# Kernel optimization log

Measured on AMD Instinct MI355X. Metric: run time of the kernel, lower is better.

## Reference

```python
import jax, jax.numpy as jnp
import numpy as np

S = 1024   # speakers_per_batch
U = 64     # utterances_per_speaker
E = 256    # model_embedding_size


def setup_inputs() -> dict:
    key = jax.random.key(0)
    k1, _ = jax.random.split(key)
    # embeds as produced by forward(): relu'd then L2-normalized rows
    raw = jax.nn.relu(jax.random.normal(k1, (S * U, E), dtype=jnp.float32))
    embeds = raw / (jnp.linalg.norm(raw, axis=1, keepdims=True) + 1e-12)
    return {
        "embeds": embeds,
        "similarity_weight": jnp.array([10.0], dtype=jnp.float32),
        "similarity_bias": jnp.array([-5.0], dtype=jnp.float32),
    }


def reference(embeds, similarity_weight, similarity_bias):
    e = embeds.reshape(S, U, E)                      # [S,U,E]
    # inclusive centroids (per speaker)
    c_incl = jnp.mean(e, axis=1)                     # [S,E]
    incl_norm = jnp.linalg.norm(c_incl, axis=1)      # [S]
    # exclusive centroids (leave-one-out per utterance)
    c_excl = (jnp.sum(e, axis=1, keepdims=True) - e) / (U - 1)  # [S,U,E]
    excl_norm = jnp.linalg.norm(c_excl, axis=2)      # [S,U]
    # off-diagonal (k != j): cosine vs inclusive centroid of speaker k
    sim = jnp.einsum('jue,ke->juk', e, c_incl) / incl_norm       # [S,U,S]
    # diagonal (k == j): cosine vs own exclusive centroid
    diag = jnp.einsum('jue,jue->ju', e, c_excl) / excl_norm      # [S,U]
    idx = jnp.arange(S)
    sim = sim.at[idx, :, idx].set(diag)
    sim = sim * similarity_weight[0] + similarity_bias[0]
    # cross-entropy against ground truth speaker ids
    logits = sim.reshape(S * U, S)                   # [SU,S]
    gt = jnp.repeat(jnp.arange(S), U)                # [SU]
    logp = jax.nn.log_softmax(logits, axis=-1)
    loss = -jnp.mean(jnp.take_along_axis(logp, gt[:, None], axis=1))
    preds = jnp.argmax(logits, axis=1)
    accuracy = jnp.mean((preds == gt).astype(jnp.float32))
    return loss, accuracy
```

## Files before the change

### kernel.cpp

```cpp
#include <hip/hip_runtime.h>
#include <math.h>

#define NS 1024
#define NU 64
#define NE 256

typedef __attribute__((ext_vector_type(4))) float f32x4;

__device__ static inline unsigned int pk4_fp8(float a, float b, float c,
                                              float d) {
  int r = 0;
  r = __builtin_amdgcn_cvt_pk_fp8_f32(a, b, r, false);
  r = __builtin_amdgcn_cvt_pk_fp8_f32(c, d, r, true);
  return (unsigned int)r;
}


__global__ __launch_bounds__(256) void centroid_kernel(
    const float* __restrict__ embeds, unsigned int* __restrict__ Cb,
    float* __restrict__ normsum, float* __restrict__ ssumG,
    unsigned int* __restrict__ pmaxG, float* __restrict__ out) {
  int k = blockIdx.x;
  int t = threadIdx.x;
  if (t < 64) {
    ssumG[k * 64 + t] = 0.f;
    pmaxG[k * 64 + t] = 0u;
  }
  int wave = t >> 6, e4 = t & 63;
  const float4* base =
      (const float4*)(embeds + (size_t)k * NU * NE) + wave * 16 * 64 + e4;
  float4 s = {0.f, 0.f, 0.f, 0.f};
#pragma unroll
  for (int i = 0; i < 16; ++i) {
    float4 v = base[i * 64];
    s.x += v.x; s.y += v.y; s.z += v.z; s.w += v.w;
  }
  __shared__ float4 ps[4][64];
  ps[wave][e4] = s;
  __syncthreads();
  if (t < 64) {
    float4 a = ps[0][t], b = ps[1][t], c = ps[2][t], d = ps[3][t];
    float4 s4;
    s4.x = a.x + b.x + c.x + d.x;
    s4.y = a.y + b.y + c.y + d.y;
    s4.z = a.z + b.z + c.z + d.z;
    s4.w = a.w + b.w + c.w + d.w;
    float sq = s4.x * s4.x + s4.y * s4.y + s4.z * s4.z + s4.w * s4.w;
#pragma unroll
    for (int off = 32; off; off >>= 1) sq += __shfl_xor(sq, off, 64);
    float nrm = sqrtf(sq);
    float inv = 1.f / nrm;
    unsigned int v = pk4_fp8(s4.x * inv, s4.y * inv, s4.z * inv, s4.w * inv);
    int idx = (k >> 4) * 1024 + (t >> 3) * 128 +
              ((((t >> 1) & 3) * 16 + (k & 15)) << 1) + (t & 1);
    Cb[idx] = v;
    if (t == 0) {
      normsum[k] = nrm;
      if (k == 0) { out[0] = 0.f; out[1] = 0.f; }
    }
  }
}

__global__ __launch_bounds__(256, 2) void main_kernel(
    const float* __restrict__ embeds, const long* __restrict__ Cb,
    const float* __restrict__ normsum, const float* __restrict__ wp,
    const float* __restrict__ bp, float* __restrict__ ssumG,
    unsigned int* __restrict__ pmaxG, float* __restrict__ pdiagG) {
  int t = threadIdx.x;
  int wave = t >> 6, lane = t & 63;
  int c = lane & 15, q = lane >> 4;
  int b = blockIdx.x;
  int rg = b >> 2;
  int hq = b & 3;
  int jspk = rg * 2 + (wave >> 1);
  int r0 = rg * 128 + wave * 32;

  float w = *wp, bia = *bp;
  const float L2E = 1.4426950408889634f;
  float M0 = fabsf(w) + bia;
  float wl = w * L2E;
  float cl = (bia - M0) * L2E;
  float ns = normsum[jspk];

  int fb = hq * 16 * 512 + lane;

  long bfA[4], bfB[4];
#pragma unroll
  for (int s = 0; s < 4; ++s) bfA[s] = Cb[fb + s * 64];
#pragma unroll
  for (int s = 0; s < 4; ++s) bfB[s] = Cb[fb + (4 + s) * 64];

  long af[2][8];
#pragma unroll
  for (int mt = 0; mt < 2; ++mt) {
    const float* rowp = embeds + (size_t)(r0 + mt * 16 + c) * NE;
#pragma unroll
    for (int s = 0; s < 8; ++s) {
      int k0 = s * 32 + q * 8;
      float4 x = *(const float4*)(rowp + k0);
      float4 y = *(const float4*)(rowp + k0 + 4);
      unsigned int lo = pk4_fp8(x.x, x.y, x.z, x.w);
      unsigned int hi = pk4_fp8(y.x, y.y, y.z, y.w);
      af[mt][s] = (long)(((unsigned long long)hi << 32) | lo);
    }
  }

  float ssum[2][4];
  float pm[2][4];
#pragma unroll
  for (int mt = 0; mt < 2; ++mt)
#pragma unroll
    for (int r = 0; r < 4; ++r) {
      ssum[mt][r] = 0.f;
      pm[mt][r] = 0.f;
    }

#pragma unroll 1
  for (int T = 0; T < 16; ++T) {
    f32x4 acc[2];
    acc[0] = (f32x4){0.f, 0.f, 0.f, 0.f};
    acc[1] = (f32x4){0.f, 0.f, 0.f, 0.f};
    int nb = fb + (T + 1) * 512;
    bool more = (T + 1 < 16);
#pragma unroll
    for (int s = 0; s < 4; ++s) {
      acc[0] = __builtin_amdgcn_mfma_f32_16x16x32_fp8_fp8(af[0][s], bfA[s],
                                                          acc[0], 0, 0, 0);
      acc[1] = __builtin_amdgcn_mfma_f32_16x16x32_fp8_fp8(af[1][s], bfA[s],
                                                          acc[1], 0, 0, 0);
    }
    if (more) {
#pragma unroll
      for (int s = 0; s < 4; ++s) bfA[s] = Cb[nb + s * 64];
    }
#pragma unroll
    for (int s = 0; s < 4; ++s) {
      acc[0] = __builtin_amdgcn_mfma_f32_16x16x32_fp8_fp8(af[0][4 + s], bfB[s],
                                                          acc[0], 0, 0, 0);
      acc[1] = __builtin_amdgcn_mfma_f32_16x16x32_fp8_fp8(af[1][4 + s], bfB[s],
                                                          acc[1], 0, 0, 0);
    }
    if (more) {
#pragma unroll
      for (int s = 0; s < 4; ++s) bfB[s] = Cb[nb + (4 + s) * 64];
    }

    int gt = hq * 16 + T;
    bool diagstep = ((jspk >> 4) == gt);
#pragma unroll
    for (int mt = 0; mt < 2; ++mt) {
      f32x4 a = acc[mt];
      if (diagstep && c == (jspk & 15)) {
#pragma unroll
        for (int r = 0; r < 4; ++r) {
          float Sv = a[r] * ns;
          float den = fmaxf(fmaf(ns, ns, 1.f) - 2.f * Sv, 1e-30f);
          float val = (Sv - 1.f) * __frsqrt_rn(den);
          float pd = exp2f(fmaf(val, wl, cl));
          pdiagG[r0 + mt * 16 + q * 4 + r] = pd;
          a[r] = val;
        }
      }
#pragma unroll
      for (int r = 0; r < 4; ++r) {
        float p = exp2f(fmaf(a[r], wl, cl));
        ssum[mt][r] += p;
        pm[mt][r] = fmaxf(pm[mt][r], p);
      }
    }
  }

#pragma unroll
  for (int mt = 0; mt < 2; ++mt)
#pragma unroll
    for (int r = 0; r < 4; ++r) {
      float s = ssum[mt][r];
      s += __shfl_xor(s, 1, 64);
      s += __shfl_xor(s, 2, 64);
      s += __shfl_xor(s, 4, 64);
      s += __shfl_xor(s, 8, 64);
      float m = pm[mt][r];
      m = fmaxf(m, __shfl_xor(m, 1, 64));
      m = fmaxf(m, __shfl_xor(m, 2, 64));
      m = fmaxf(m, __shfl_xor(m, 4, 64));
      m = fmaxf(m, __shfl_xor(m, 8, 64));
      if (c == 0) {
        int row = r0 + mt * 16 + q * 4 + r;
        atomicAdd(&ssumG[row], s);
        atomicMax(&pmaxG[row], __float_as_uint(m));
      }
    }
}

__global__ __launch_bounds__(256) void reduce_kernel(
    const float* __restrict__ ssumG, const unsigned int* __restrict__ pmaxG,
    const float* __restrict__ pdiagG, float* __restrict__ out) {
  int i = blockIdx.x * 256 + threadIdx.x;
  float pd = pdiagG[i];
  float lossr = __logf(ssumG[i] / pd);
  float corr = (pd >= __uint_as_float(pmaxG[i])) ? 1.f : 0.f;
#pragma unroll
  for (int off = 32; off; off >>= 1) {
    lossr += __shfl_xor(lossr, off, 64);
    corr += __shfl_xor(corr, off, 64);
  }
  __shared__ float pl[4], pc[4];
  int wave = threadIdx.x >> 6, lane = threadIdx.x & 63;
  if (lane == 0) { pl[wave] = lossr; pc[wave] = corr; }
  __syncthreads();
  if (threadIdx.x == 0) {
    const float inv = 1.f / (float)(NS * NU);
    atomicAdd(&out[0], (pl[0] + pl[1] + pl[2] + pl[3]) * inv);
    atomicAdd(&out[1], (pc[0] + pc[1] + pc[2] + pc[3]) * inv);
  }
}

extern "C" void kernel_launch(void* const* d_in, const int* in_sizes, int n_in,
                              void* d_out, int out_size, void* d_ws,
                              size_t ws_size, hipStream_t stream) {
  const float* embeds = (const float*)d_in[0];
  const float* w = (const float*)d_in[1];
  const float* b = (const float*)d_in[2];
  float* out = (float*)d_out;
  char* ws = (char*)d_ws;
  unsigned int* Cb = (unsigned int*)ws;
  unsigned int* pmaxG = (unsigned int*)(ws + (256 << 10));
  float* ssumG = (float*)(ws + (512 << 10));
  float* pdiagG = (float*)(ws + (768 << 10));
  float* normsum = (float*)(ws + (1024 << 10));

  centroid_kernel<<<NS, 256, 0, stream>>>(embeds, Cb, normsum, ssumG, pmaxG,
                                          out);
  main_kernel<<<2048, 256, 0, stream>>>(embeds, (const long*)Cb, normsum, w, b,
                                        ssumG, pmaxG, pdiagG);
  reduce_kernel<<<NS * NU / 256, 256, 0, stream>>>(ssumG, pmaxG, pdiagG, out);
}
```

Before: 164.5 us.

## Pre-pack embeddings to fp8 fragments in centroid kernel, halve main grid

The centroid kernel now also converts each speaker's embedding rows into fp8 MFMA A-fragments and stores them in a packed workspace buffer. The main kernel loads these ready-made fragments instead of reading fp32 rows and converting them. Its grid also drops from 2048 to 1024 blocks, each covering 32 column tiles instead of 16. This cuts the redundant fp32 reads and conversions that were repeated across four blocks per row group, at the cost of an extra fp8 write and read pass and less parallelism in the main kernel.

```diff
diff --git a/kernel.cpp b/kernel.cpp
--- a/kernel.cpp
+++ b/kernel.cpp
@@ -18,8 +18,9 @@
 
 __global__ __launch_bounds__(256) void centroid_kernel(
     const float* __restrict__ embeds, unsigned int* __restrict__ Cb,
-    float* __restrict__ normsum, float* __restrict__ ssumG,
-    unsigned int* __restrict__ pmaxG, float* __restrict__ out) {
+    unsigned long long* __restrict__ Ab, float* __restrict__ normsum,
+    float* __restrict__ ssumG, unsigned int* __restrict__ pmaxG,
+    float* __restrict__ out) {
   int k = blockIdx.x;
   int t = threadIdx.x;
   if (t < 64) {
@@ -27,6 +28,7 @@
     pmaxG[k * 64 + t] = 0u;
   }
   int wave = t >> 6, e4 = t & 63;
+
   const float4* base =
       (const float4*)(embeds + (size_t)k * NU * NE) + wave * 16 * 64 + e4;
   float4 s = {0.f, 0.f, 0.f, 0.f};
@@ -59,10 +61,27 @@
       if (k == 0) { out[0] = 0.f; out[1] = 0.f; }
     }
   }
+
+  {
+    int tile = t >> 6;
+    int l = t & 63;
+    int m = l & 15, qq = l >> 4;
+    const float* rowp = embeds + (size_t)(k * 64 + tile * 16 + m) * NE;
+    size_t basei = ((size_t)k * 4 + tile) * 512 + l;
+#pragma unroll
+    for (int sI = 0; sI < 8; ++sI) {
+      int k0 = sI * 32 + qq * 8;
+      float4 x = *(const float4*)(rowp + k0);
+      float4 y = *(const float4*)(rowp + k0 + 4);
+      unsigned int lo = pk4_fp8(x.x, x.y, x.z, x.w);
+      unsigned int hi = pk4_fp8(y.x, y.y, y.z, y.w);
+      Ab[basei + sI * 64] = ((unsigned long long)hi << 32) | lo;
+    }
+  }
 }
 
 __global__ __launch_bounds__(256, 2) void main_kernel(
-    const float* __restrict__ embeds, const long* __restrict__ Cb,
+    const long* __restrict__ Ab, const long* __restrict__ Cb,
     const float* __restrict__ normsum, const float* __restrict__ wp,
     const float* __restrict__ bp, float* __restrict__ ssumG,
     unsigned int* __restrict__ pmaxG, float* __restrict__ pdiagG) {
@@ -70,8 +89,8 @@
   int wave = t >> 6, lane = t & 63;
   int c = lane & 15, q = lane >> 4;
   int b = blockIdx.x;
-  int rg = b >> 2;
-  int hq = b & 3;
+  int rg = b >> 1;
+  int h = b & 1;
   int jspk = rg * 2 + (wave >> 1);
   int r0 = rg * 128 + wave * 32;
 
@@ -82,7 +101,7 @@
   float cl = (bia - M0) * L2E;
   float ns = normsum[jspk];
 
-  int fb = hq * 16 * 512 + lane;
+  int fb = h * 32 * 512 + lane;
 
   long bfA[4], bfB[4];
 #pragma unroll
@@ -93,16 +112,9 @@
   long af[2][8];
 #pragma unroll
   for (int mt = 0; mt < 2; ++mt) {
-    const float* rowp = embeds + (size_t)(r0 + mt * 16 + c) * NE;
-#pragma unroll
-    for (int s = 0; s < 8; ++s) {
-      int k0 = s * 32 + q * 8;
-      float4 x = *(const float4*)(rowp + k0);
-      float4 y = *(const float4*)(rowp + k0 + 4);
-      unsigned int lo = pk4_fp8(x.x, x.y, x.z, x.w);
-      unsigned int hi = pk4_fp8(y.x, y.y, y.z, y.w);
-      af[mt][s] = (long)(((unsigned long long)hi << 32) | lo);
-    }
+    int ab = ((r0 >> 4) + mt) * 512 + lane;
+#pragma unroll
+    for (int s = 0; s < 8; ++s) af[mt][s] = Ab[ab + s * 64];
   }
 
   float ssum[2][4];
@@ -116,12 +128,12 @@
     }
 
 #pragma unroll 1
-  for (int T = 0; T < 16; ++T) {
+  for (int T = 0; T < 32; ++T) {
     f32x4 acc[2];
     acc[0] = (f32x4){0.f, 0.f, 0.f, 0.f};
     acc[1] = (f32x4){0.f, 0.f, 0.f, 0.f};
     int nb = fb + (T + 1) * 512;
-    bool more = (T + 1 < 16);
+    bool more = (T + 1 < 32);
 #pragma unroll
     for (int s = 0; s < 4; ++s) {
       acc[0] = __builtin_amdgcn_mfma_f32_16x16x32_fp8_fp8(af[0][s], bfA[s],
@@ -145,7 +157,7 @@
       for (int s = 0; s < 4; ++s) bfB[s] = Cb[nb + (4 + s) * 64];
     }
 
-    int gt = hq * 16 + T;
+    int gt = h * 32 + T;
     bool diagstep = ((jspk >> 4) == gt);
 #pragma unroll
     for (int mt = 0; mt < 2; ++mt) {
@@ -228,10 +240,12 @@
   float* ssumG = (float*)(ws + (512 << 10));
   float* pdiagG = (float*)(ws + (768 << 10));
   float* normsum = (float*)(ws + (1024 << 10));
-
-  centroid_kernel<<<NS, 256, 0, stream>>>(embeds, Cb, normsum, ssumG, pmaxG,
-                                          out);
-  main_kernel<<<2048, 256, 0, stream>>>(embeds, (const long*)Cb, normsum, w, b,
-                                        ssumG, pmaxG, pdiagG);
+  unsigned long long* Ab =
+      (unsigned long long*)(ws + (1056 << 10));
+
+  centroid_kernel<<<NS, 256, 0, stream>>>(embeds, Cb, Ab, normsum, ssumG,
+                                          pmaxG, out);
+  main_kernel<<<1024, 256, 0, stream>>>((const long*)Ab, (const long*)Cb,
+                                        normsum, w, b, ssumG, pmaxG, pdiagG);
   reduce_kernel<<<NS * NU / 256, 256, 0, stream>>>(ssumG, pmaxG, pdiagG, out);
 }
```

Result: faster. 149.8 us (-8.9%).
